# Kernel tuning notes

Measured on AMD Instinct MI355X. Metric: run time of the kernel, lower is better.

## Reference

```python
import jax, jax.numpy as jnp
import numpy as np

THRESHOLD = 1.0  # snntorch Leaky default


def _heaviside(u):
    return (u > 0).astype(u.dtype)


def _leaky_step(cur, mem_prev, beta):
    # snntorch Leaky (reset_mechanism='subtract'):
    #   reset based on PREVIOUS membrane, then integrate, then fire
    reset = _heaviside(mem_prev - THRESHOLD)
    mem = beta * mem_prev + cur - reset * THRESHOLD
    spk = _heaviside(mem - THRESHOLD)
    return spk, mem


def setup_inputs() -> dict:
    key = jax.random.key(0)
    ks = jax.random.split(key, 5)
    B, n_inp, n_hid, n_out = 16384, 1024, 4096, 4
    x = jax.random.normal(ks[0], (B, n_inp), dtype=jnp.float32)
    W1 = jax.random.normal(ks[1], (n_hid, n_inp), dtype=jnp.float32) * (1.0 / np.sqrt(n_inp))
    b1 = jax.random.normal(ks[2], (n_hid,), dtype=jnp.float32) * 0.01
    W2 = jax.random.normal(ks[3], (n_out, n_hid), dtype=jnp.float32) * (1.0 / np.sqrt(n_hid))
    b2 = jax.random.normal(ks[4], (n_out,), dtype=jnp.float32) * 0.01
    beta = jnp.float32(0.9)
    return {"x": x, "W1": W1, "b1": b1, "W2": W2, "b2": b2, "beta": beta}


def reference(x, W1, b1, W2, b2, beta):
    # forward does x.unsqueeze(1) -> time dim of size 1, so exactly one LIF step
    # with zero-initialized membranes (init_leaky()).
    B = x.shape[0]
    mem1 = jnp.zeros((B, W1.shape[0]), dtype=x.dtype)
    mem2 = jnp.zeros((B, W2.shape[0]), dtype=x.dtype)

    cur1 = x @ W1.T + b1                      # [B, n_hid]
    spk1, mem1 = _leaky_step(cur1, mem1, beta)
    cur2 = spk1 @ W2.T + b2                   # [B, 4]
    spk2, mem2 = _leaky_step(cur2, mem2, beta)

    # original returns (mem2_rec, spk2_rec) as length-1 lists per timestep
    return mem2, spk2
```

## Files before the change

kernel.cpp:

```cpp
#include <hip/hip_runtime.h>
#include <cstdint>
#include <cstddef>

typedef __attribute__((ext_vector_type(8))) _Float16 f16x8;
typedef __attribute__((ext_vector_type(4))) float f32x4;

#define B_ROWS 16384
#define K_DIM  1024
#define H_DIM  4096
#define O_DIM  4
#define NT     32
#define MARGIN 2.5e-3f
#define STASH_CAP 2048

#define OFF_XH   ((size_t)0)
#define OFF_WH   ((size_t)33554432)
#define OFF_BITS ((size_t)41943040)
#define WS_NEED  ((size_t)50331648)

#define GLD16(g, l) __builtin_amdgcn_global_load_lds(                         \
    (const __attribute__((address_space(1))) void*)(g),                       \
    (__attribute__((address_space(3))) void*)(l), 16, 0, 0)

__global__ __launch_bounds__(256) void split_f16(
    const float* __restrict__ x, const float* __restrict__ W1,
    _Float16* __restrict__ Xh, _Float16* __restrict__ Wh)
{
    const int NX8 = (B_ROWS * K_DIM) / 8;
    const int NW8 = (H_DIM * K_DIM) / 8;
    const int stride = gridDim.x * blockDim.x;
    for (int i = blockIdx.x * blockDim.x + threadIdx.x; i < NX8 + NW8; i += stride) {
        const float* src; _Float16* dst; int j;
        if (i < NX8) { src = x; dst = Xh; j = i; }
        else         { src = W1; dst = Wh; j = i - NX8; }
        const float4 f0 = reinterpret_cast<const float4*>(src)[2 * j];
        const float4 f1 = reinterpret_cast<const float4*>(src)[2 * j + 1];
        f16x8 h;
        h[0] = (_Float16)f0.x; h[1] = (_Float16)f0.y;
        h[2] = (_Float16)f0.z; h[3] = (_Float16)f0.w;
        h[4] = (_Float16)f1.x; h[5] = (_Float16)f1.y;
        h[6] = (_Float16)f1.z; h[7] = (_Float16)f1.w;
        reinterpret_cast<f16x8*>(dst)[j] = h;
    }
}

__global__ __launch_bounds__(512, 4) void fc1_f16(
    const _Float16* __restrict__ Xh, const _Float16* __restrict__ Wh,
    const float* __restrict__ xf, const float* __restrict__ w1f,
    const float* __restrict__ b1, uint32_t* __restrict__ bits)
{
    __shared__ __align__(16) _Float16 As[3][256 * 32];
    __shared__ __align__(16) _Float16 Bs[3][128 * 32];
    __shared__ uint32_t scnt;

    const int tid  = threadIdx.x;
    const int lane = tid & 63;
    const int w    = tid >> 6;
    const int m0   = blockIdx.y * 256;
    const int n0   = blockIdx.x * 128;

    const int   srow   = w * 16 + (lane >> 2);
    const int   schunk = (((lane & 3) ^ ((srow >> 1) & 3)) << 3);
    const size_t gA0 = (size_t)(m0 + srow) * K_DIM + schunk;
    const size_t gA1 = (size_t)(m0 + 128 + srow) * K_DIM + schunk;
    const size_t gB0 = (size_t)(n0 + srow) * K_DIM + schunk;

    auto stage = [&](int rb, int t) {
        const int k0 = t * 32;
        GLD16(Xh + gA0 + k0, &As[rb][w * 512]);
        GLD16(Xh + gA1 + k0, &As[rb][4096 + w * 512]);
        GLD16(Wh + gB0 + k0, &Bs[rb][w * 512]);
    };

    const int wr   = (w >> 1) * 64;
    const int wc   = (w & 1) * 64;
    const int frow = lane & 15;
    const int rsw  = (((lane >> 4) ^ ((frow >> 1) & 3)) << 3);

    f32x4 acc[4][4];
#pragma unroll
    for (int i = 0; i < 4; ++i)
#pragma unroll
        for (int j = 0; j < 4; ++j)
            acc[i][j] = (f32x4){0.f, 0.f, 0.f, 0.f};

    stage(0, 0);
    stage(1, 1);
    asm volatile("s_waitcnt vmcnt(3)" ::: "memory");
    __builtin_amdgcn_s_barrier();

    int cur = 0, s2 = 2;
    for (int t = 0; t < NT; ++t) {
        if (t + 2 < NT) stage(s2, t + 2);
        f16x8 a[4], b[4];
#pragma unroll
        for (int mi = 0; mi < 4; ++mi)
            a[mi] = *reinterpret_cast<const f16x8*>(
                &As[cur][(wr + mi * 16 + frow) * 32 + rsw]);
#pragma unroll
        for (int nj = 0; nj < 4; ++nj)
            b[nj] = *reinterpret_cast<const f16x8*>(
                &Bs[cur][(wc + nj * 16 + frow) * 32 + rsw]);
#pragma unroll
        for (int mi = 0; mi < 4; ++mi)
#pragma unroll
            for (int nj = 0; nj < 4; ++nj)
                acc[mi][nj] = __builtin_amdgcn_mfma_f32_16x16x32_f16(
                    a[mi], b[nj], acc[mi][nj], 0, 0, 0);
        asm volatile("s_waitcnt lgkmcnt(0)" ::: "memory");
        if (t + 2 < NT) { asm volatile("s_waitcnt vmcnt(3)" ::: "memory"); }
        else            { asm volatile("s_waitcnt vmcnt(0)" ::: "memory"); }
        __builtin_amdgcn_s_barrier();
        cur = (cur == 2) ? 0 : cur + 1;
        s2  = (s2  == 2) ? 0 : s2  + 1;
    }

    __syncthreads();
    uint32_t* stash  = (uint32_t*)&As[0][0];
    uint32_t* bitbuf = (uint32_t*)&Bs[0][0];
    if (tid == 0) scnt = 0u;
    __syncthreads();

    float bcol[4];
#pragma unroll
    for (int nj = 0; nj < 4; ++nj) bcol[nj] = b1[n0 + wc + nj * 16 + frow];

    const int g = lane >> 4;
#pragma unroll
    for (int mi = 0; mi < 4; ++mi) {
#pragma unroll
        for (int r = 0; r < 4; ++r) {
            unsigned long long bj[4];
#pragma unroll
            for (int nj = 0; nj < 4; ++nj) {
                const float cur_v = acc[mi][nj][r] + bcol[nj];
                bj[nj] = __ballot(cur_v > 1.0f);
                if (fabsf(cur_v - 1.0f) < MARGIN) {
                    const uint32_t enc =
                        ((uint32_t)(wr + mi * 16 + g * 4 + r) << 7)
                      | (uint32_t)(wc + nj * 16 + frow);
                    uint32_t ix = atomicAdd(&scnt, 1u);
                    if (ix < STASH_CAP) stash[ix] = enc;
                }
            }
            if (frow == 0) {
                const int row_l = wr + mi * 16 + g * 4 + r;
                const uint32_t w0 =
                    (uint32_t)((bj[0] >> (g * 16)) & 0xFFFFull) |
                    ((uint32_t)((bj[1] >> (g * 16)) & 0xFFFFull) << 16);
                const uint32_t w1 =
                    (uint32_t)((bj[2] >> (g * 16)) & 0xFFFFull) |
                    ((uint32_t)((bj[3] >> (g * 16)) & 0xFFFFull) << 16);
                uint2 v; v.x = w0; v.y = w1;
                *reinterpret_cast<uint2*>(&bitbuf[row_l * 4 + (wc >> 5)]) = v;
            }
        }
    }
    __syncthreads();

    const uint32_t nf = (scnt < STASH_CAP) ? scnt : STASH_CAP;
    for (uint32_t f = (uint32_t)w; f < nf; f += 8) {
        const uint32_t e = stash[f];
        const int row_l = (int)(e >> 7), col_l = (int)(e & 127);
        const float4* xr  = (const float4*)(xf  + (size_t)(m0 + row_l) * K_DIM);
        const float4* wr2 = (const float4*)(w1f + (size_t)(n0 + col_l) * K_DIM);
        double s = 0.0;
#pragma unroll
        for (int i = 0; i < 4; ++i) {
            const float4 xa = xr[lane + i * 64];
            const float4 wa = wr2[lane + i * 64];
            s = fma((double)xa.x, (double)wa.x, s);
            s = fma((double)xa.y, (double)wa.y, s);
            s = fma((double)xa.z, (double)wa.z, s);
            s = fma((double)xa.w, (double)wa.w, s);
        }
        for (int off = 32; off; off >>= 1) s += __shfl_down(s, off, 64);
        if (lane == 0) {
            const double cur_v = s + (double)b1[n0 + col_l];
            uint32_t* word = &bitbuf[row_l * 4 + (col_l >> 5)];
            const uint32_t mask = 1u << (col_l & 31);
            if (cur_v > 1.0) atomicOr(word, mask);
            else             atomicAnd(word, ~mask);
        }
    }
    __syncthreads();

    if (tid < 256) {
        const uint4 v = *reinterpret_cast<const uint4*>(&bitbuf[tid * 4]);
        *reinterpret_cast<uint4*>(
            &bits[(size_t)(m0 + tid) * 128 + (n0 >> 5)]) = v;
    }
}

__global__ __launch_bounds__(256) void fc2w4(
    const uint32_t* __restrict__ bits, const float* __restrict__ W2,
    const float* __restrict__ b2, float* __restrict__ out)
{
    const int lane = threadIdx.x & 63;
    const int rb   = (blockIdx.x * 4 + (threadIdx.x >> 6)) * 4;
    uint32_t w0[4], w1[4];
#pragma unroll
    for (int rr = 0; rr < 4; ++rr) {
        const uint2 v = *reinterpret_cast<const uint2*>(
            &bits[(size_t)(rb + rr) * 128 + 2 * lane]);
        w0[rr] = v.x; w1[rr] = v.y;
    }
    double acc[4][4];
#pragma unroll
    for (int rr = 0; rr < 4; ++rr)
#pragma unroll
        for (int o = 0; o < 4; ++o) acc[rr][o] = 0.0;

#pragma unroll
    for (int o = 0; o < 4; ++o) {
        const float4* wrow = (const float4*)(W2 + (size_t)o * H_DIM + lane * 64);
#pragma unroll
        for (int q = 0; q < 16; ++q) {
            const float4 v = wrow[q];
            const int bit = (4 * q) & 31;
#pragma unroll
            for (int rr = 0; rr < 4; ++rr) {
                const uint32_t word = (q < 8) ? w0[rr] : w1[rr];
                if ((word >> bit)       & 1u) acc[rr][o] += (double)v.x;
                if ((word >> (bit + 1)) & 1u) acc[rr][o] += (double)v.y;
                if ((word >> (bit + 2)) & 1u) acc[rr][o] += (double)v.z;
                if ((word >> (bit + 3)) & 1u) acc[rr][o] += (double)v.w;
            }
        }
    }
#pragma unroll
    for (int off = 32; off; off >>= 1)
#pragma unroll
        for (int rr = 0; rr < 4; ++rr)
#pragma unroll
            for (int o = 0; o < 4; ++o)
                acc[rr][o] += __shfl_down(acc[rr][o], off, 64);
    if (lane == 0) {
#pragma unroll
        for (int rr = 0; rr < 4; ++rr)
#pragma unroll
            for (int o = 0; o < 4; ++o) {
                const double cur = acc[rr][o] + (double)b2[o];
                out[(rb + rr) * 4 + o] = (float)cur;
                out[B_ROWS * O_DIM + (rb + rr) * 4 + o] = (cur > 1.0) ? 1.0f : 0.0f;
            }
    }
}

#define BM 64
#define BN 64
#define BK 32
__global__ __launch_bounds__(256) void snn_fc1(
    const float* __restrict__ x, const float* __restrict__ W1,
    const float* __restrict__ b1, uint32_t* __restrict__ spk_bits)
{
    __shared__ float As[BK][68];
    __shared__ float Bs[BK][68];
    __shared__ uint32_t bitbuf[BM][BN / 32];

    const int tid = threadIdx.x;
    const int m0 = blockIdx.y * BM;
    const int n0 = blockIdx.x * BN;
    const int rm = tid & 15, cn = tid >> 4;
    const int mf = 4 * rm, nf = 4 * cn;

    double acc[4][4];
#pragma unroll
    for (int i = 0; i < 4; ++i)
#pragma unroll
        for (int j = 0; j < 4; ++j) acc[i][j] = 0.0;

    const int sm = tid >> 3, skq = tid & 7;
    for (int kt = 0; kt < K_DIM / BK; ++kt) {
        const int k0 = kt * BK;
#pragma unroll
        for (int s = 0; s < 2; ++s) {
            const int m = sm + 32 * s;
            const float4 av = *reinterpret_cast<const float4*>(
                x + (size_t)(m0 + m) * K_DIM + k0 + 4 * skq);
            As[4 * skq + 0][m] = av.x; As[4 * skq + 1][m] = av.y;
            As[4 * skq + 2][m] = av.z; As[4 * skq + 3][m] = av.w;
            const float4 bv = *reinterpret_cast<const float4*>(
                W1 + (size_t)(n0 + m) * K_DIM + k0 + 4 * skq);
            Bs[4 * skq + 0][m] = bv.x; Bs[4 * skq + 1][m] = bv.y;
            Bs[4 * skq + 2][m] = bv.z; Bs[4 * skq + 3][m] = bv.w;
        }
        __syncthreads();
#pragma unroll
        for (int k = 0; k < BK; ++k) {
            const float4 af = *reinterpret_cast<const float4*>(&As[k][mf]);
            const float4 bf = *reinterpret_cast<const float4*>(&Bs[k][nf]);
            const double a0 = af.x, a1 = af.y, a2 = af.z, a3 = af.w;
            const double b0 = bf.x, b1v = bf.y, b2v = bf.z, b3 = bf.w;
            acc[0][0] = fma(a0, b0, acc[0][0]);  acc[0][1] = fma(a0, b1v, acc[0][1]);
            acc[0][2] = fma(a0, b2v, acc[0][2]); acc[0][3] = fma(a0, b3, acc[0][3]);
            acc[1][0] = fma(a1, b0, acc[1][0]);  acc[1][1] = fma(a1, b1v, acc[1][1]);
            acc[1][2] = fma(a1, b2v, acc[1][2]); acc[1][3] = fma(a1, b3, acc[1][3]);
            acc[2][0] = fma(a2, b0, acc[2][0]);  acc[2][1] = fma(a2, b1v, acc[2][1]);
            acc[2][2] = fma(a2, b2v, acc[2][2]); acc[2][3] = fma(a2, b3, acc[2][3]);
            acc[3][0] = fma(a3, b0, acc[3][0]);  acc[3][1] = fma(a3, b1v, acc[3][1]);
            acc[3][2] = fma(a3, b2v, acc[3][2]); acc[3][3] = fma(a3, b3, acc[3][3]);
        }
        __syncthreads();
    }

    if (tid < BM * (BN / 32)) bitbuf[tid >> 1][tid & 1] = 0u;
    __syncthreads();
#pragma unroll
    for (int j = 0; j < 4; ++j) {
        const int n = nf + j;
        const double bias = (double)b1[n0 + n];
        const int wd = n >> 5, bit = n & 31;
#pragma unroll
        for (int i = 0; i < 4; ++i) {
            const double cur = acc[i][j] + bias;
            if (cur > 1.0) atomicOr(&bitbuf[mf + i][wd], 1u << bit);
        }
    }
    __syncthreads();
    if (tid < 128) {
        const int r = tid >> 1, wd = tid & 1;
        spk_bits[(size_t)(m0 + r) * (H_DIM / 32) + (n0 >> 5) + wd] = bitbuf[r][wd];
    }
}

extern "C" void kernel_launch(void* const* d_in, const int* in_sizes, int n_in,
                              void* d_out, int out_size, void* d_ws, size_t ws_size,
                              hipStream_t stream) {
    const float* x  = (const float*)d_in[0];
    const float* W1 = (const float*)d_in[1];
    const float* b1 = (const float*)d_in[2];
    const float* W2 = (const float*)d_in[3];
    const float* b2 = (const float*)d_in[4];
    float* out = (float*)d_out;
    char* ws = (char*)d_ws;

    if (ws_size >= WS_NEED) {
        _Float16* Xh   = (_Float16*)(ws + OFF_XH);
        _Float16* Wh   = (_Float16*)(ws + OFF_WH);
        uint32_t* bits = (uint32_t*)(ws + OFF_BITS);

        split_f16<<<4096, 256, 0, stream>>>(x, W1, Xh, Wh);
        fc1_f16<<<dim3(H_DIM / 128, B_ROWS / 256), 512, 0, stream>>>(
            Xh, Wh, x, W1, b1, bits);
        fc2w4<<<B_ROWS / 16, 256, 0, stream>>>(bits, W2, b2, out);
    } else {
        uint32_t* bits = (uint32_t*)ws;
        dim3 g1(H_DIM / BN, B_ROWS / BM);
        snn_fc1<<<g1, 256, 0, stream>>>(x, W1, b1, bits);
        fc2w4<<<B_ROWS / 16, 256, 0, stream>>>(bits, W2, b2, out);
    }
}
```

Measured before the change: 263.6 us.

## Rewrite fc1 GEMM as 256x256 tile with 8-phase ping-pong pipeline

Replaces the 256x128, K=32, triple-buffered fc1 main loop with a 256x256 tile and K=64 steps. The loop is double-buffered and split into eight phases per iteration, each interleaving LDS fragment reads, global-to-LDS prefetch of the next A/B halves, barriers, and MFMA bursts wrapped in s_setprio. The larger tile raises arithmetic intensity and halves re-reads of X. The phased schedule aims to overlap memory traffic with matrix math. In exchange, the per-thread accumulator count doubles, occupancy drops to 2 blocks per CU, LDS use grows, and the epilogue stash encoding and bit-buffer layout change to fit 256 columns.

```diff
diff --git a/kernel.cpp b/kernel.cpp
--- a/kernel.cpp
+++ b/kernel.cpp
@@ -9,7 +9,6 @@
 #define K_DIM  1024
 #define H_DIM  4096
 #define O_DIM  4
-#define NT     32
 #define MARGIN 2.5e-3f
 #define STASH_CAP 2048
 
@@ -44,75 +43,116 @@
     }
 }
 
-__global__ __launch_bounds__(512, 4) void fc1_f16(
+#define BAR    __builtin_amdgcn_s_barrier()
+#define LGKM0  asm volatile("s_waitcnt lgkmcnt(0)" ::: "memory")
+#define VMC4   asm volatile("s_waitcnt vmcnt(4)" ::: "memory")
+#define VMC0   asm volatile("s_waitcnt vmcnt(0)" ::: "memory")
+#define PRIO1  __builtin_amdgcn_s_setprio(1)
+#define PRIO0  __builtin_amdgcn_s_setprio(0)
+
+#define RDA(DB, Q, AFR) do {                                                  \
+  _Pragma("unroll") for (int i_ = 0; i_ < 2; ++i_)                            \
+  _Pragma("unroll") for (int kk_ = 0; kk_ < 2; ++kk_) {                       \
+    const int row_ = (wm << 7) + ((Q) * 2 + i_) * 16 + frow;                  \
+    const int ch_  = (kk_ * 4 + fkc) ^ ((row_ >> 1) & 7);                     \
+    AFR[i_][kk_] = *reinterpret_cast<const f16x8*>(                           \
+        &As[DB][row_ * 64 + ch_ * 8]); }                                      \
+} while (0)
+
+#define RDB(DB, BFR) do {                                                     \
+  _Pragma("unroll") for (int nj_ = 0; nj_ < 4; ++nj_)                         \
+  _Pragma("unroll") for (int kk_ = 0; kk_ < 2; ++kk_) {                       \
+    const int row_ = (wn << 6) + nj_ * 16 + frow;                             \
+    const int ch_  = (kk_ * 4 + fkc) ^ ((row_ >> 1) & 7);                     \
+    BFR[nj_][kk_] = *reinterpret_cast<const f16x8*>(                          \
+        &Bs[DB][row_ * 64 + ch_ * 8]); }                                      \
+} while (0)
+
+#define MM16(Q, AFR, BFR) do {                                                \
+  _Pragma("unroll") for (int i_ = 0; i_ < 2; ++i_)                            \
+  _Pragma("unroll") for (int nj_ = 0; nj_ < 4; ++nj_)                         \
+  _Pragma("unroll") for (int kk_ = 0; kk_ < 2; ++kk_)                         \
+    acc[(Q) * 2 + i_][nj_] = __builtin_amdgcn_mfma_f32_16x16x32_f16(          \
+        AFR[i_][kk_], BFR[nj_][kk_], acc[(Q) * 2 + i_][nj_], 0, 0, 0);        \
+} while (0)
+
+__global__ __launch_bounds__(512, 2) void fc1_8ph(
     const _Float16* __restrict__ Xh, const _Float16* __restrict__ Wh,
     const float* __restrict__ xf, const float* __restrict__ w1f,
     const float* __restrict__ b1, uint32_t* __restrict__ bits)
 {
-    __shared__ __align__(16) _Float16 As[3][256 * 32];
-    __shared__ __align__(16) _Float16 Bs[3][128 * 32];
+    __shared__ __align__(16) _Float16 As[2][256 * 64];
+    __shared__ __align__(16) _Float16 Bs[2][256 * 64];
     __shared__ uint32_t scnt;
 
     const int tid  = threadIdx.x;
     const int lane = tid & 63;
     const int w    = tid >> 6;
+    const int wm   = w >> 2;
+    const int wn   = w & 3;
     const int m0   = blockIdx.y * 256;
-    const int n0   = blockIdx.x * 128;
-
-    const int   srow   = w * 16 + (lane >> 2);
-    const int   schunk = (((lane & 3) ^ ((srow >> 1) & 3)) << 3);
-    const size_t gA0 = (size_t)(m0 + srow) * K_DIM + schunk;
-    const size_t gA1 = (size_t)(m0 + 128 + srow) * K_DIM + schunk;
-    const size_t gB0 = (size_t)(n0 + srow) * K_DIM + schunk;
-
-    auto stage = [&](int rb, int t) {
-        const int k0 = t * 32;
-        GLD16(Xh + gA0 + k0, &As[rb][w * 512]);
-        GLD16(Xh + gA1 + k0, &As[rb][4096 + w * 512]);
-        GLD16(Wh + gB0 + k0, &Bs[rb][w * 512]);
+    const int n0   = blockIdx.x * 256;
+    const int frow = lane & 15;
+    const int fkc  = lane >> 4;
+
+    const int sr8 = (w << 3) + (lane >> 3);
+    const int sc  = lane & 7;
+
+    auto stA = [&](int db, int kt, int half) {
+#pragma unroll
+        for (int c = 0; c < 2; ++c) {
+            const int rw  = half * 128 + c * 64 + sr8;
+            const int gch = sc ^ ((rw >> 1) & 7);
+            GLD16(Xh + (size_t)(m0 + rw) * K_DIM + kt * 64 + gch * 8,
+                  &As[db][(half * 128 + c * 64 + (w << 3)) * 64]);
+        }
     };
-
-    const int wr   = (w >> 1) * 64;
-    const int wc   = (w & 1) * 64;
-    const int frow = lane & 15;
-    const int rsw  = (((lane >> 4) ^ ((frow >> 1) & 3)) << 3);
-
-    f32x4 acc[4][4];
-#pragma unroll
-    for (int i = 0; i < 4; ++i)
+    auto stB = [&](int db, int kt, int half) {
+#pragma unroll
+        for (int c = 0; c < 2; ++c) {
+            const int rw  = half * 128 + c * 64 + sr8;
+            const int gch = sc ^ ((rw >> 1) & 7);
+            GLD16(Wh + (size_t)(n0 + rw) * K_DIM + kt * 64 + gch * 8,
+                  &Bs[db][(half * 128 + c * 64 + (w << 3)) * 64]);
+        }
+    };
+
+    f32x4 acc[8][4];
+#pragma unroll
+    for (int i = 0; i < 8; ++i)
 #pragma unroll
         for (int j = 0; j < 4; ++j)
             acc[i][j] = (f32x4){0.f, 0.f, 0.f, 0.f};
 
-    stage(0, 0);
-    stage(1, 1);
-    asm volatile("s_waitcnt vmcnt(3)" ::: "memory");
-    __builtin_amdgcn_s_barrier();
-
-    int cur = 0, s2 = 2;
-    for (int t = 0; t < NT; ++t) {
-        if (t + 2 < NT) stage(s2, t + 2);
-        f16x8 a[4], b[4];
-#pragma unroll
-        for (int mi = 0; mi < 4; ++mi)
-            a[mi] = *reinterpret_cast<const f16x8*>(
-                &As[cur][(wr + mi * 16 + frow) * 32 + rsw]);
-#pragma unroll
-        for (int nj = 0; nj < 4; ++nj)
-            b[nj] = *reinterpret_cast<const f16x8*>(
-                &Bs[cur][(wc + nj * 16 + frow) * 32 + rsw]);
-#pragma unroll
-        for (int mi = 0; mi < 4; ++mi)
-#pragma unroll
-            for (int nj = 0; nj < 4; ++nj)
-                acc[mi][nj] = __builtin_amdgcn_mfma_f32_16x16x32_f16(
-                    a[mi], b[nj], acc[mi][nj], 0, 0, 0);
-        asm volatile("s_waitcnt lgkmcnt(0)" ::: "memory");
-        if (t + 2 < NT) { asm volatile("s_waitcnt vmcnt(3)" ::: "memory"); }
-        else            { asm volatile("s_waitcnt vmcnt(0)" ::: "memory"); }
-        __builtin_amdgcn_s_barrier();
-        cur = (cur == 2) ? 0 : cur + 1;
-        s2  = (s2  == 2) ? 0 : s2  + 1;
+    stA(0, 0, 0); stA(0, 0, 1); stB(0, 0, 0); stB(0, 0, 1);
+    stB(1, 1, 0); stB(1, 1, 1);
+    VMC4; BAR;
+
+#pragma unroll 1
+    for (int it = 0; it < 8; ++it) {
+        const int ktA1 = 2 * it + 1, ktN = 2 * it + 2, ktN2 = 2 * it + 3;
+        const bool more = (it < 7);
+        f16x8 bfr[4][2], afr[2][2];
+
+        RDB(0, bfr); RDA(0, 0, afr);
+        stA(1, ktA1, 0); stA(1, ktA1, 1);
+        BAR; LGKM0; PRIO1; MM16(0, afr, bfr); PRIO0; BAR;
+        RDA(0, 1, afr); if (more) stB(0, ktN, 0);
+        BAR; LGKM0; PRIO1; MM16(1, afr, bfr); PRIO0; BAR;
+        RDA(0, 2, afr); if (more) stB(0, ktN, 1);
+        BAR; LGKM0; PRIO1; MM16(2, afr, bfr); PRIO0; BAR;
+        RDA(0, 3, afr);
+        BAR; LGKM0; PRIO1; MM16(3, afr, bfr); PRIO0; VMC4; BAR;
+        RDB(1, bfr); RDA(1, 0, afr); if (more) stA(0, ktN, 0);
+        BAR; LGKM0; PRIO1; MM16(0, afr, bfr); PRIO0; BAR;
+        RDA(1, 1, afr); if (more) stA(0, ktN, 1);
+        BAR; LGKM0; PRIO1; MM16(1, afr, bfr); PRIO0; BAR;
+        RDA(1, 2, afr); if (more) stB(1, ktN2, 0);
+        BAR; LGKM0; PRIO1; MM16(2, afr, bfr); PRIO0; BAR;
+        RDA(1, 3, afr); if (more) stB(1, ktN2, 1);
+        BAR; LGKM0; PRIO1; MM16(3, afr, bfr); PRIO0;
+        if (more) { VMC4; } else { VMC0; }
+        BAR;
     }
 
     __syncthreads();
@@ -123,11 +163,11 @@
 
     float bcol[4];
 #pragma unroll
-    for (int nj = 0; nj < 4; ++nj) bcol[nj] = b1[n0 + wc + nj * 16 + frow];
+    for (int nj = 0; nj < 4; ++nj) bcol[nj] = b1[n0 + (wn << 6) + nj * 16 + frow];
 
     const int g = lane >> 4;
 #pragma unroll
-    for (int mi = 0; mi < 4; ++mi) {
+    for (int mi = 0; mi < 8; ++mi) {
 #pragma unroll
         for (int r = 0; r < 4; ++r) {
             unsigned long long bj[4];
@@ -137,14 +177,14 @@
                 bj[nj] = __ballot(cur_v > 1.0f);
                 if (fabsf(cur_v - 1.0f) < MARGIN) {
                     const uint32_t enc =
-                        ((uint32_t)(wr + mi * 16 + g * 4 + r) << 7)
-                      | (uint32_t)(wc + nj * 16 + frow);
+                        ((uint32_t)((wm << 7) + mi * 16 + g * 4 + r) << 8)
+                      | (uint32_t)((wn << 6) + nj * 16 + frow);
                     uint32_t ix = atomicAdd(&scnt, 1u);
                     if (ix < STASH_CAP) stash[ix] = enc;
                 }
             }
             if (frow == 0) {
-                const int row_l = wr + mi * 16 + g * 4 + r;
+                const int row_l = (wm << 7) + mi * 16 + g * 4 + r;
                 const uint32_t w0 =
                     (uint32_t)((bj[0] >> (g * 16)) & 0xFFFFull) |
                     ((uint32_t)((bj[1] >> (g * 16)) & 0xFFFFull) << 16);
@@ -152,7 +192,7 @@
                     (uint32_t)((bj[2] >> (g * 16)) & 0xFFFFull) |
                     ((uint32_t)((bj[3] >> (g * 16)) & 0xFFFFull) << 16);
                 uint2 v; v.x = w0; v.y = w1;
-                *reinterpret_cast<uint2*>(&bitbuf[row_l * 4 + (wc >> 5)]) = v;
+                *reinterpret_cast<uint2*>(&bitbuf[row_l * 8 + (wn << 1)]) = v;
             }
         }
     }
@@ -161,7 +201,7 @@
     const uint32_t nf = (scnt < STASH_CAP) ? scnt : STASH_CAP;
     for (uint32_t f = (uint32_t)w; f < nf; f += 8) {
         const uint32_t e = stash[f];
-        const int row_l = (int)(e >> 7), col_l = (int)(e & 127);
+        const int row_l = (int)(e >> 8), col_l = (int)(e & 255);
         const float4* xr  = (const float4*)(xf  + (size_t)(m0 + row_l) * K_DIM);
         const float4* wr2 = (const float4*)(w1f + (size_t)(n0 + col_l) * K_DIM);
         double s = 0.0;
@@ -177,7 +217,7 @@
         for (int off = 32; off; off >>= 1) s += __shfl_down(s, off, 64);
         if (lane == 0) {
             const double cur_v = s + (double)b1[n0 + col_l];
-            uint32_t* word = &bitbuf[row_l * 4 + (col_l >> 5)];
+            uint32_t* word = &bitbuf[row_l * 8 + (col_l >> 5)];
             const uint32_t mask = 1u << (col_l & 31);
             if (cur_v > 1.0) atomicOr(word, mask);
             else             atomicAnd(word, ~mask);
@@ -185,10 +225,11 @@
     }
     __syncthreads();
 
-    if (tid < 256) {
-        const uint4 v = *reinterpret_cast<const uint4*>(&bitbuf[tid * 4]);
+    {
+        const int row = tid >> 1, qw = tid & 1;
+        const uint4 v = *reinterpret_cast<const uint4*>(&bitbuf[row * 8 + qw * 4]);
         *reinterpret_cast<uint4*>(
-            &bits[(size_t)(m0 + tid) * 128 + (n0 >> 5)]) = v;
+            &bits[(size_t)(m0 + row) * 128 + (n0 >> 5) + qw * 4]) = v;
     }
 }
 
@@ -341,7 +382,7 @@
         uint32_t* bits = (uint32_t*)(ws + OFF_BITS);
 
         split_f16<<<4096, 256, 0, stream>>>(x, W1, Xh, Wh);
-        fc1_f16<<<dim3(H_DIM / 128, B_ROWS / 256), 512, 0, stream>>>(
+        fc1_8ph<<<dim3(H_DIM / 256, B_ROWS / 256), 512, 0, stream>>>(
             Xh, Wh, x, W1, b1, bits);
         fc2w4<<<B_ROWS / 16, 256, 0, stream>>>(bits, W2, b2, out);
     } else {
```

Result: faster. 256.7 us (-2.6%).
